# Performance work log

Measured on AMD Instinct MI355X. Metric: run time of the kernel, lower is better.

Reference implementation:

```python
import jax, jax.numpy as jnp
import numpy as np

N_HEAD = 12

def setup_inputs() -> dict:
    key = jax.random.key(0)
    k1, k2, k3 = jax.random.split(key, 3)
    B, T, C = 8, 1024, 768
    x = jax.random.normal(k1, (B, T, C), dtype=jnp.float32)
    # torch Linear(768, 3*768): store as [in, out] so we can do x @ W
    W_attn = jax.random.normal(k2, (C, 3 * C), dtype=jnp.float32) * 0.02
    b_attn = jax.random.normal(k3, (3 * C,), dtype=jnp.float32) * 0.02
    return {"x": x, "W_attn": W_attn, "b_attn": b_attn}

def reference(x, W_attn, b_attn):
    B, T, C = x.shape
    H = N_HEAD
    hs = C // H
    scale = 1.0 / jnp.sqrt(jnp.asarray(hs, dtype=x.dtype))
    qkv = x @ W_attn + b_attn                      # [B,T,3C]
    q, k, v = jnp.split(qkv, 3, axis=-1)
    q = q.reshape(B, T, H, hs).transpose(0, 2, 1, 3)  # [B,H,T,hs]
    k = k.reshape(B, T, H, hs).transpose(0, 2, 1, 3)
    v = v.reshape(B, T, H, hs).transpose(0, 2, 1, 3)
    scores = jnp.einsum('bhqd,bhkd->bhqk', q, k) * scale
    # causal mask then ReLU (masked -inf entries become 0 after ReLU)
    causal = jnp.tril(jnp.ones((T, T), dtype=bool))
    att = jnp.where(causal[None, None], jax.nn.relu(scores), jnp.zeros((), dtype=scores.dtype))
    out = jnp.einsum('bhqk,bhkd->bhqd', att, v)    # [B,H,T,hs]
    out = out.transpose(0, 2, 1, 3).reshape(B, T, C)
    return out
```

## Files before the change

kernel.cpp:

```cpp
#include <hip/hip_runtime.h>

typedef __attribute__((ext_vector_type(8))) short bf16x8;
typedef __attribute__((ext_vector_type(4))) float f32x4;
typedef __attribute__((ext_vector_type(4))) unsigned short us4;
typedef __attribute__((ext_vector_type(8))) unsigned short us8;

#define MFMA(a, b, c) __builtin_amdgcn_mfma_f32_16x16x32_bf16((a), (b), (c), 0, 0, 0)

__device__ __forceinline__ unsigned short f2bf(float f) {
  unsigned u = __builtin_bit_cast(unsigned, f);
  u = (u + 0x7fffu + ((u >> 16) & 1u)) >> 16;
  return (unsigned short)u;
}

__device__ __forceinline__ void gload16(const void* g, void* l) {
  __builtin_amdgcn_global_load_lds((const __attribute__((address_space(1))) void*)g,
                                   (__attribute__((address_space(3))) void*)l,
                                   16, 0, 0);
}

__device__ __forceinline__ bf16x8 readfrag(const unsigned short* buf, int row, int kbyte) {
  int byte = row * 128 + kbyte;
  byte ^= (row & 7) << 4;
  return *(const bf16x8*)((const char*)buf + byte);
}

__global__ void cast_x_kernel(const float* __restrict__ x,
                              unsigned short* __restrict__ xb, int n4) {
  int id = blockIdx.x * blockDim.x + threadIdx.x;
  if (id >= n4) return;
  float4 v = ((const float4*)x)[id];
  us4 o = { f2bf(v.x), f2bf(v.y), f2bf(v.z), f2bf(v.w) };
  ((us4*)xb)[id] = o;
}

__global__ void castw_kernel(const float* __restrict__ W,
                             unsigned short* __restrict__ Wt) {
  __shared__ unsigned short tile[32][33];
  int bn = blockIdx.x * 32;
  int bk = blockIdx.y * 32;
  int lx = threadIdx.x & 31, ly = threadIdx.x >> 5;
#pragma unroll
  for (int i = 0; i < 32; i += 8)
    tile[ly + i][lx] = f2bf(W[(bk + ly + i) * 2304 + bn + lx]);
  __syncthreads();
#pragma unroll
  for (int i = 0; i < 32; i += 8)
    Wt[(bn + ly + i) * 768 + bk + lx] = tile[lx][ly + i];
}

__global__ __launch_bounds__(256, 2) void qkv_gemm_kernel(
    const unsigned short* __restrict__ xb, const unsigned short* __restrict__ wt,
    const float* __restrict__ bias,
    unsigned short* __restrict__ qb, unsigned short* __restrict__ kb,
    unsigned short* __restrict__ vb) {
  __shared__ unsigned short lds[40960];
  const int tid = threadIdx.x;
  const int lane = tid & 63, wid = tid >> 6;
  const int wm = wid >> 1, wn = wid & 1;
  const int l15 = lane & 15, lg = lane >> 4;

  int bid = blockIdx.x;
  int xcd = bid & 7, c = bid >> 3;
  int mb = xcd * 8 + (c & 7);
  int nb = c >> 3;
  const int m0 = mb * 128, n0 = nb * 128;

  const unsigned short* Ab_g = xb + (size_t)m0 * 768;
  const unsigned short* Bb_g = wt + (size_t)n0 * 768;

  int eA[4], sA[4];
#pragma unroll
  for (int i = 0; i < 4; ++i) {
    int e = (i * 256 + tid) * 8, row = e >> 6;
    eA[i] = e;
    sA[i] = row * 768 + ((e ^ ((row & 7) << 3)) & 63);
  }

#define SA(buf, k0, i) gload16(Ab_g + sA[i] + (k0), &lds[(buf) * 8192 + eA[i]])
#define SB(buf, k0, i) gload16(Bb_g + sA[i] + (k0), &lds[24576 + (buf) * 8192 + eA[i]])

  f32x4 acc[4][4] = {};
  bf16x8 bfr[4][2];

  SA(0, 0, 0); SA(0, 0, 1); SA(0, 0, 2); SA(0, 0, 3);
  SB(0, 0, 0); SB(0, 0, 1); SB(0, 0, 2); SB(0, 0, 3);
  SA(1, 64, 0); SA(1, 64, 1); SA(1, 64, 2); SA(1, 64, 3);
  asm volatile("s_waitcnt vmcnt(4)" ::: "memory");
  __builtin_amdgcn_s_barrier();

#define GPHASE(cA_, cB_, P, STG, EW)                                              \
  {                                                                               \
    const unsigned short* Abuf = &lds[(cA_) * 8192];                              \
    const unsigned short* Bbuf = &lds[24576 + (cB_) * 8192];                      \
    bf16x8 afr[2][2];                                                             \
    _Pragma("unroll") for (int m2 = 0; m2 < 2; ++m2)                              \
        _Pragma("unroll") for (int kk = 0; kk < 2; ++kk)                          \
            afr[m2][kk] =                                                         \
        readfrag(Abuf, wm * 64 + ((P) * 2 + m2) * 16 + l15, kk * 64 + lg * 16);   \
    if ((P) == 0) {                                                               \
      _Pragma("unroll") for (int nf = 0; nf < 4; ++nf)                            \
          _Pragma("unroll") for (int kk = 0; kk < 2; ++kk)                        \
              bfr[nf][kk] =                                                       \
          readfrag(Bbuf, wn * 64 + nf * 16 + l15, kk * 64 + lg * 16);             \
    }                                                                             \
    STG;                                                                          \
    __builtin_amdgcn_sched_barrier(0);                                            \
    __builtin_amdgcn_s_barrier();                                                 \
    asm volatile("s_waitcnt lgkmcnt(0)" ::: "memory");                            \
    __builtin_amdgcn_sched_barrier(0);                                            \
    __builtin_amdgcn_s_setprio(1);                                                \
    _Pragma("unroll") for (int m2 = 0; m2 < 2; ++m2)                              \
        _Pragma("unroll") for (int nf = 0; nf < 4; ++nf)                          \
            _Pragma("unroll") for (int kk = 0; kk < 2; ++kk)                      \
                acc[(P) * 2 + m2][nf] =                                           \
        MFMA(afr[m2][kk], bfr[nf][kk], acc[(P) * 2 + m2][nf]);                    \
    __builtin_amdgcn_s_setprio(0);                                                \
    EW;                                                                           \
    __builtin_amdgcn_sched_barrier(0);                                            \
    __builtin_amdgcn_s_barrier();                                                 \
  }

  int cA = 0;
  for (int t = 0; t < 10; ++t) {
    int cB = t & 1, cBn = cB ^ 1;
    int cA2 = cA + 2; if (cA2 >= 3) cA2 -= 3;
    int k1 = (t + 1) * 64, k2 = (t + 2) * 64;
    GPHASE(cA, cB, 0, { SB(cBn, k1, 0); SB(cBn, k1, 1); SB(cBn, k1, 2); SB(cBn, k1, 3); }, );
    GPHASE(cA, cB, 1, { SA(cA2, k2, 0); SA(cA2, k2, 1); SA(cA2, k2, 2); SA(cA2, k2, 3); },
           asm volatile("s_waitcnt vmcnt(4)" ::: "memory"));
    cA = (cA == 2) ? 0 : cA + 1;
  }
  GPHASE(cA, 0, 0, { SB(1, 704, 0); SB(1, 704, 1); SB(1, 704, 2); SB(1, 704, 3); }, );
  GPHASE(cA, 0, 1, , asm volatile("s_waitcnt vmcnt(0)" ::: "memory"));
  cA = (cA == 2) ? 0 : cA + 1;
  GPHASE(cA, 1, 0, , );
  GPHASE(cA, 1, 1, , );

  __syncthreads();

  const int sec = n0 / 768;
  float bcol[4];
#pragma unroll
  for (int nf = 0; nf < 4; ++nf) bcol[nf] = bias[n0 + wn * 64 + nf * 16 + l15];

  if (sec < 2) {
    unsigned short* ct = lds;
#pragma unroll
    for (int mf = 0; mf < 4; ++mf)
#pragma unroll
      for (int nf = 0; nf < 4; ++nf)
#pragma unroll
        for (int r = 0; r < 4; ++r)
          ct[(wm * 64 + mf * 16 + lg * 4 + r) * 128 + wn * 64 + nf * 16 + l15] =
              f2bf(acc[mf][nf][r] + bcol[nf]);
    __syncthreads();
    unsigned short* dstbase = (sec == 0) ? qb : kb;
    const int hbase = (n0 - sec * 768) >> 6;
    const int g8 = tid >> 3, l8 = tid & 7;
#pragma unroll
    for (int j = 0; j < 8; ++j) {
      int chunk = j * 32 + g8;
      int row = chunk >> 1, hh = chunk & 1;
      us8 v = *(const us8*)&ct[row * 128 + hh * 64 + l8 * 8];
      int t = m0 + row, bb = t >> 10, tt = t & 1023;
      *(us8*)(dstbase + ((size_t)((bb * 12 + hbase + hh) * 1024 + tt)) * 64 + l8 * 8) = v;
    }
  } else {
#pragma unroll
    for (int nf = 0; nf < 4; ++nf) {
      int cc2 = (n0 - 1536) + wn * 64 + nf * 16 + l15;
      int h = cc2 >> 6, d = cc2 & 63;
#pragma unroll
      for (int mf = 0; mf < 4; ++mf) {
        int row0 = m0 + wm * 64 + mf * 16 + lg * 4;
        int bb = row0 >> 10, t0 = row0 & 1023;
        us4 o;
#pragma unroll
        for (int r = 0; r < 4; ++r) o[r] = f2bf(acc[mf][nf][r] + bcol[nf]);
        *(us4*)(vb + ((size_t)((bb * 12 + h) * 64 + d)) * 1024 + t0) = o;
      }
    }
  }
#undef SA
#undef SB
#undef GPHASE
}

__global__ __launch_bounds__(512, 2) void attn_kernel(
    const unsigned short* __restrict__ qb, const unsigned short* __restrict__ kb,
    const unsigned short* __restrict__ vb, float* __restrict__ out) {
  __shared__ unsigned short lds[65536];
  const int tid = threadIdx.x;
  const int lane = tid & 63, wid = tid >> 6;
  const int qs = wid >> 1, ks = wid & 1;
  const int l15 = lane & 15, lg = lane >> 4;

  int bid = blockIdx.x;
  int xcd = bid & 7, c = bid >> 3;
  int bh = xcd * 12 + (c % 12);
  int byq = 3 - (c / 12);
  const int b = bh / 12, h = bh % 12;
  const size_t base = (size_t)bh * 65536;
  const int Q = byq * 4 + qs;
  const int qr0 = byq * 256 + qs * 64;

  bf16x8 aq[4][2];
#pragma unroll
  for (int mf = 0; mf < 4; ++mf)
#pragma unroll
    for (int kk = 0; kk < 2; ++kk)
      aq[mf][kk] = *(const bf16x8*)(qb + base + (size_t)(qr0 + mf * 16 + l15) * 64 +
                                    kk * 32 + lg * 8);

  const int e = tid * 8;
  const int row = e >> 6;
  const int esw = e ^ ((row & 7) << 3);

#define ASTAGE(buf, i_)                                                            \
  {                                                                                \
    int kt0 = 2 * (i_);                                                            \
    gload16(kb + base + (size_t)kt0 * 4096 + esw, &lds[(buf) * 8192 + e]);         \
    gload16(kb + base + (size_t)(kt0 + 1) * 4096 + esw,                            \
            &lds[(buf) * 8192 + 4096 + e]);                                        \
    gload16(vb + base + (size_t)row * 1024 + kt0 * 64 + (esw & 63),                \
            &lds[16384 + (buf) * 8192 + e]);                                       \
    gload16(vb + base + (size_t)row * 1024 + (kt0 + 1) * 64 + (esw & 63),          \
            &lds[16384 + (buf) * 8192 + 4096 + e]);                                \
  }

  f32x4 o[4][4] = {};
  unsigned short* Sb = &lds[32768 + wid * 4096];

  const int niter = 2 * byq + 2;
  ASTAGE(0, 0);
  asm volatile("s_waitcnt vmcnt(0)" ::: "memory");
  __builtin_amdgcn_s_barrier();

  for (int i = 0; i < niter; ++i) {
    const int cur = i & 1;
    if (i + 1 < niter) ASTAGE(cur ^ 1, i + 1);
    const int kt = 2 * i + ks;
    if (kt <= Q) {
      const unsigned short* Kb = &lds[cur * 8192 + ks * 4096];
      const unsigned short* Vb = &lds[16384 + cur * 8192 + ks * 4096];
      bf16x8 bk[4][2];
#pragma unroll
      for (int nf = 0; nf < 4; ++nf)
#pragma unroll
        for (int kk = 0; kk < 2; ++kk)
          bk[nf][kk] = readfrag(Kb, nf * 16 + l15, kk * 64 + lg * 16);
      const bool diag = (kt == Q);
      __builtin_amdgcn_s_setprio(1);
#pragma unroll
      for (int mf = 0; mf < 4; ++mf)
#pragma unroll
        for (int nf = 0; nf < 4; ++nf) {
          f32x4 s = {};
          s = MFMA(aq[mf][0], bk[nf][0], s);
          s = MFMA(aq[mf][1], bk[nf][1], s);
          int colk = nf * 16 + l15;
#pragma unroll
          for (int r = 0; r < 4; ++r) {
            int rowq = mf * 16 + lg * 4 + r;
            float v = fmaxf(s[r] * 0.125f, 0.0f);
            if (diag && colk > rowq) v = 0.0f;
            int byte = (rowq * 128 + colk * 2) ^ ((rowq & 7) << 4);
            *(unsigned short*)((char*)Sb + byte) = f2bf(v);
          }
        }
      __builtin_amdgcn_s_setprio(0);
      bf16x8 pa[4][2];
#pragma unroll
      for (int mf = 0; mf < 4; ++mf)
#pragma unroll
        for (int kk = 0; kk < 2; ++kk)
          pa[mf][kk] = readfrag(Sb, mf * 16 + l15, kk * 64 + lg * 16);
      __builtin_amdgcn_s_setprio(1);
#pragma unroll
      for (int mf = 0; mf < 4; ++mf)
#pragma unroll
        for (int df = 0; df < 4; ++df)
#pragma unroll
          for (int kk = 0; kk < 2; ++kk)
            o[mf][df] = MFMA(pa[mf][kk], readfrag(Vb, df * 16 + l15, kk * 64 + lg * 16),
                             o[mf][df]);
      __builtin_amdgcn_s_setprio(0);
    }
    asm volatile("s_waitcnt vmcnt(0)" ::: "memory");
    __builtin_amdgcn_sched_barrier(0);
    __builtin_amdgcn_s_barrier();
  }
#undef ASTAGE

  float* fr = (float*)lds;
  if (ks == 1) {
#pragma unroll
    for (int mf = 0; mf < 4; ++mf)
#pragma unroll
      for (int df = 0; df < 4; ++df)
#pragma unroll
        for (int r = 0; r < 4; ++r) {
          int rowq = mf * 16 + lg * 4 + r, col = df * 16 + l15;
          int idx = (qs * 4096 + rowq * 64 + col) ^ ((rowq & 4) << 2);
          fr[idx] = o[mf][df][r];
        }
  }
  __syncthreads();
  if (ks == 0) {
#pragma unroll
    for (int mf = 0; mf < 4; ++mf)
#pragma unroll
      for (int df = 0; df < 4; ++df)
#pragma unroll
        for (int r = 0; r < 4; ++r) {
          int rowq = mf * 16 + lg * 4 + r, col = df * 16 + l15;
          int idx = (qs * 4096 + rowq * 64 + col) ^ ((rowq & 4) << 2);
          float v = o[mf][df][r] + fr[idx];
          out[(size_t)(b * 1024 + qr0 + rowq) * 768 + h * 64 + col] = v;
        }
  }
}

extern "C" void kernel_launch(void* const* d_in, const int* in_sizes, int n_in,
                              void* d_out, int out_size, void* d_ws, size_t ws_size,
                              hipStream_t stream) {
  const float* x = (const float*)d_in[0];
  const float* W = (const float*)d_in[1];
  const float* bias = (const float*)d_in[2];
  float* out = (float*)d_out;

  unsigned short* xb = (unsigned short*)d_ws;
  unsigned short* wt = xb + 6291456;
  unsigned short* qb = wt + 1769472;
  unsigned short* kb = qb + 6291456;
  unsigned short* vb = kb + 6291456;

  cast_x_kernel<<<6144, 256, 0, stream>>>(x, xb, 1572864);
  castw_kernel<<<dim3(72, 24), 256, 0, stream>>>(W, wt);
  qkv_gemm_kernel<<<1152, 256, 0, stream>>>(xb, wt, bias, qb, kb, vb);
  attn_kernel<<<384, 512, 0, stream>>>(qb, kb, vb, out);
}
```

Before: 87.00 us.

## Swap QK MFMA operands to write packed S rows, fold scale into Q

Swaps the A/B operands of the QK^T MFMA so each lane holds four consecutive key columns for one query row. The score tile can then be written to LDS as one 8-byte store using the hardware packed bf16 convert, instead of four scalar 2-byte stores with software rounding. The 1/sqrt(hs) scale is folded into Q during the projection epilogue, which removes a multiply per score. The packed convert's rounding may differ slightly from the manual rounding, and pre-scaling Q changes where bf16 rounding happens.

```diff
diff --git a/kernel.cpp b/kernel.cpp
--- a/kernel.cpp
+++ b/kernel.cpp
@@ -11,6 +11,12 @@
   unsigned u = __builtin_bit_cast(unsigned, f);
   u = (u + 0x7fffu + ((u >> 16) & 1u)) >> 16;
   return (unsigned short)u;
+}
+
+__device__ __forceinline__ unsigned cvt_pk_bf16(float lo, float hi) {
+  unsigned r;
+  asm("v_cvt_pk_bf16_f32 %0, %1, %2" : "=v"(r) : "v"(lo), "v"(hi));
+  return r;
 }
 
 __device__ __forceinline__ void gload16(const void* g, void* l) {
@@ -140,6 +146,7 @@
   __syncthreads();
 
   const int sec = n0 / 768;
+  const float qs = (sec == 0) ? 0.125f : 1.0f;
   float bcol[4];
 #pragma unroll
   for (int nf = 0; nf < 4; ++nf) bcol[nf] = bias[n0 + wn * 64 + nf * 16 + l15];
@@ -153,7 +160,7 @@
 #pragma unroll
         for (int r = 0; r < 4; ++r)
           ct[(wm * 64 + mf * 16 + lg * 4 + r) * 128 + wn * 64 + nf * 16 + l15] =
-              f2bf(acc[mf][nf][r] + bcol[nf]);
+              f2bf((acc[mf][nf][r] + bcol[nf]) * qs);
     __syncthreads();
     unsigned short* dstbase = (sec == 0) ? qb : kb;
     const int hbase = (n0 - sec * 768) >> 6;
@@ -257,17 +264,27 @@
 #pragma unroll
         for (int nf = 0; nf < 4; ++nf) {
           f32x4 s = {};
-          s = MFMA(aq[mf][0], bk[nf][0], s);
-          s = MFMA(aq[mf][1], bk[nf][1], s);
-          int colk = nf * 16 + l15;
-#pragma unroll
-          for (int r = 0; r < 4; ++r) {
-            int rowq = mf * 16 + lg * 4 + r;
-            float v = fmaxf(s[r] * 0.125f, 0.0f);
-            if (diag && colk > rowq) v = 0.0f;
-            int byte = (rowq * 128 + colk * 2) ^ ((rowq & 7) << 4);
-            *(unsigned short*)((char*)Sb + byte) = f2bf(v);
+          s = MFMA(bk[nf][0], aq[mf][0], s);
+          s = MFMA(bk[nf][1], aq[mf][1], s);
+          float v0, v1, v2, v3;
+          if (diag) {
+            int q = mf * 16 + l15, k0 = nf * 16 + lg * 4;
+            v0 = (k0 + 0 <= q) ? fmaxf(s[0], 0.0f) : 0.0f;
+            v1 = (k0 + 1 <= q) ? fmaxf(s[1], 0.0f) : 0.0f;
+            v2 = (k0 + 2 <= q) ? fmaxf(s[2], 0.0f) : 0.0f;
+            v3 = (k0 + 3 <= q) ? fmaxf(s[3], 0.0f) : 0.0f;
+          } else {
+            v0 = fmaxf(s[0], 0.0f);
+            v1 = fmaxf(s[1], 0.0f);
+            v2 = fmaxf(s[2], 0.0f);
+            v3 = fmaxf(s[3], 0.0f);
           }
+          uint2 w;
+          w.x = cvt_pk_bf16(v0, v1);
+          w.y = cvt_pk_bf16(v2, v3);
+          int rowq = mf * 16 + l15;
+          int byte = (rowq * 128 + (nf * 16 + lg * 4) * 2) ^ ((rowq & 7) << 4);
+          *(uint2*)((char*)Sb + byte) = w;
         }
       __builtin_amdgcn_s_setprio(0);
       bf16x8 pa[4][2];
```

Result: faster. 84.09 us (-3.3%).
